# Performance work log

Hardware: AMD Instinct MI355X
Metric: run time of the kernel (lower is better)

Reference implementation:

```python
import jax, jax.numpy as jnp
import numpy as np

NEG = -1e9
CLIP = 10.0  # tanh clipping constant for SingleHeadAttention logits


def layer_norm(x, g, b, eps=1e-5):
    mu = jnp.mean(x, axis=-1, keepdims=True)
    var = jnp.var(x, axis=-1, keepdims=True)
    return (x - mu) * jax.lax.rsqrt(var + eps) * g + b


def setup_inputs() -> dict:
    key = jax.random.key(0)
    ks = jax.random.split(key, 16)
    B, A, N, E, Hf = 4096, 16, 128, 128, 128
    s = 0.02
    inp = {
        "agent_embed": jax.random.normal(ks[0], (B, A, E), jnp.float32),
        "city_embed": jax.random.normal(ks[1], (B, N, E), jnp.float32),
        "acts": jax.random.randint(ks[2], (B, A), 0, N, jnp.int32),
        # cross-attention layer params
        "Wq": jax.random.normal(ks[3], (E, E), jnp.float32) * s,
        "Wk": jax.random.normal(ks[4], (E, E), jnp.float32) * s,
        "Wv": jax.random.normal(ks[5], (E, E), jnp.float32) * s,
        "Wo": jax.random.normal(ks[6], (E, E), jnp.float32) * s,
        "ln1_g": jnp.ones((E,), jnp.float32),
        "ln1_b": jnp.zeros((E,), jnp.float32),
        "W1": jax.random.normal(ks[7], (E, Hf), jnp.float32) * s,
        "b1": jnp.zeros((Hf,), jnp.float32),
        "W2": jax.random.normal(ks[8], (Hf, E), jnp.float32) * s,
        "b2": jnp.zeros((E,), jnp.float32),
        "ln2_g": jnp.ones((E,), jnp.float32),
        "ln2_b": jnp.zeros((E,), jnp.float32),
        # single-head attention params
        "Wq_s": jax.random.normal(ks[9], (E, E), jnp.float32) * s,
        "Wk_s": jax.random.normal(ks[10], (E, E), jnp.float32) * s,
    }
    return inp


def reference(agent_embed, city_embed, acts, Wq, Wk, Wv, Wo, ln1_g, ln1_b,
              W1, b1, W2, b2, ln2_g, ln2_b, Wq_s, Wk_s):
    B, A, E = agent_embed.shape
    H = 8
    dh = E // H

    # ---- conflict mask construction ----
    eq = acts[:, :, None] == acts[:, None, :]            # [B,A,A] True = same city
    ident = jnp.eye(A, dtype=bool)[None]                 # [1,A,A]
    conflict = jnp.where(acts[:, :, None] == 0, ident, eq)
    mask = ~conflict                                     # True = blocked in attention

    # ---- gather per-agent selected city embeddings ----
    selected = jnp.take_along_axis(city_embed, acts[:, :, None].astype(jnp.int32), axis=1)  # [B,A,E]

    # ---- cross-attention layer (num_layers = 1) ----
    cac = selected
    q = (cac @ Wq).reshape(B, A, H, dh)
    k = (agent_embed @ Wk).reshape(B, A, H, dh)
    v = (agent_embed @ Wv).reshape(B, A, H, dh)
    scores = jnp.einsum("bqhd,bkhd->bhqk", q, k) / np.sqrt(dh).astype(np.float32)
    scores = jnp.where(mask[:, None, :, :], NEG, scores)
    attn = jax.nn.softmax(scores, axis=-1)
    out = jnp.einsum("bhqk,bkhd->bqhd", attn, v).reshape(B, A, E) @ Wo
    h = layer_norm(cac + out, ln1_g, ln1_b)
    ffn = jax.nn.relu(h @ W1 + b1) @ W2 + b2
    cac = layer_norm(h + ffn, ln2_g, ln2_b)

    # ---- single-head attention producing logits [B,A,A] ----
    qs = cac @ Wq_s
    ks_ = agent_embed @ Wk_s
    logits = jnp.einsum("bqe,bke->bqk", qs, ks_) / np.sqrt(E).astype(np.float32)
    logits = CLIP * jnp.tanh(logits)
    logits = jnp.where(mask, NEG, logits)
    return logits
```

## Files before the change

kernel.cpp:

```cpp
#include <hip/hip_runtime.h>
#include <hip/hip_bf16.h>
#include <math.h>

typedef __attribute__((ext_vector_type(8))) short bfrag;
typedef __attribute__((ext_vector_type(4))) short short4v;
typedef __attribute__((ext_vector_type(4))) float f32x4;

#define LDK 136


static __device__ __forceinline__ float b2f(short s)
{
    unsigned int u = ((unsigned int)(unsigned short)s) << 16;
    float f;
    __builtin_memcpy(&f, &u, 4);
    return f;
}

__global__ __launch_bounds__(256) void prep_weights(
    const float* __restrict__ Wq, const float* __restrict__ Wk,
    const float* __restrict__ Wv, const float* __restrict__ Wo,
    const float* __restrict__ W1, const float* __restrict__ W2,
    const float* __restrict__ Wqs, const float* __restrict__ Wks,
    __hip_bfloat16* __restrict__ out)
{
    __shared__ __hip_bfloat16 t[128 * 17];
    const float* Ws[8] = {Wq, Wk, Wv, Wo, W1, W2, Wqs, Wks};
    const int mat = blockIdx.x >> 3;
    const int slab = blockIdx.x & 7;
    const float* W = Ws[mat];
    const int n0 = slab * 16;
    __hip_bfloat16* o = out + (size_t)mat * 16384 + (size_t)n0 * 128;

#pragma unroll
    for (int p = 0; p < 2; ++p) {
        int idx = p * 256 + threadIdx.x;
        int k = idx >> 2, c4 = idx & 3;
        float4 f = *(const float4*)(W + k * 128 + n0 + c4 * 4);
        __hip_bfloat16* d = t + k * 17 + c4 * 4;
        d[0] = __float2bfloat16(f.x); d[1] = __float2bfloat16(f.y);
        d[2] = __float2bfloat16(f.z); d[3] = __float2bfloat16(f.w);
    }
    __syncthreads();
    {
        int n = threadIdx.x >> 4;
        int k0 = (threadIdx.x & 15) * 8;
        __hip_bfloat16 v[8];
#pragma unroll
        for (int j = 0; j < 8; ++j) v[j] = t[(k0 + j) * 17 + n];
        *(bfrag*)(o + n * 128 + k0) = *(const bfrag*)v;
    }
}

__device__ __forceinline__ void mm_accT(const __hip_bfloat16* X,
                                        const __hip_bfloat16* __restrict__ wT,
                                        int m, int quad, int ct0, f32x4 acc[2][2])
{
    const f32x4 z = {0.f, 0.f, 0.f, 0.f};
    acc[0][0] = z; acc[0][1] = z; acc[1][0] = z; acc[1][1] = z;
#pragma unroll
    for (int kk = 0; kk < 128; kk += 32) {
        const int k = kk + quad * 8;
        bfrag x0 = *(const bfrag*)(X + m * LDK + k);
        bfrag x1 = *(const bfrag*)(X + (16 + m) * LDK + k);
        bfrag w0 = *(const bfrag*)(wT + (size_t)(ct0 * 16 + m) * 128 + k);
        bfrag w1 = *(const bfrag*)(wT + (size_t)((ct0 + 1) * 16 + m) * 128 + k);
        acc[0][0] = __builtin_amdgcn_mfma_f32_16x16x32_bf16(w0, x0, acc[0][0], 0, 0, 0);
        acc[1][0] = __builtin_amdgcn_mfma_f32_16x16x32_bf16(w0, x1, acc[1][0], 0, 0, 0);
        acc[0][1] = __builtin_amdgcn_mfma_f32_16x16x32_bf16(w1, x0, acc[0][1], 0, 0, 0);
        acc[1][1] = __builtin_amdgcn_mfma_f32_16x16x32_bf16(w1, x1, acc[1][1], 0, 0, 0);
    }
}

__device__ __forceinline__ void mm_acc(const __hip_bfloat16* A,
                                       const __hip_bfloat16* __restrict__ wT,
                                       int m, int quad, int ct0, f32x4 acc[2][2])
{
    const f32x4 z = {0.f, 0.f, 0.f, 0.f};
    acc[0][0] = z; acc[0][1] = z; acc[1][0] = z; acc[1][1] = z;
#pragma unroll
    for (int kk = 0; kk < 128; kk += 32) {
        const int k = kk + quad * 8;
        bfrag a0 = *(const bfrag*)(A + m * LDK + k);
        bfrag a1 = *(const bfrag*)(A + (16 + m) * LDK + k);
        bfrag b0 = *(const bfrag*)(wT + (size_t)(ct0 * 16 + m) * 128 + k);
        bfrag b1 = *(const bfrag*)(wT + (size_t)((ct0 + 1) * 16 + m) * 128 + k);
        acc[0][0] = __builtin_amdgcn_mfma_f32_16x16x32_bf16(a0, b0, acc[0][0], 0, 0, 0);
        acc[1][0] = __builtin_amdgcn_mfma_f32_16x16x32_bf16(a1, b0, acc[1][0], 0, 0, 0);
        acc[0][1] = __builtin_amdgcn_mfma_f32_16x16x32_bf16(a0, b1, acc[0][1], 0, 0, 0);
        acc[1][1] = __builtin_amdgcn_mfma_f32_16x16x32_bf16(a1, b1, acc[1][1], 0, 0, 0);
    }
}

__device__ __forceinline__ void store_t(__hip_bfloat16* dst, f32x4 acc[2][2],
                                        int m, int quad, int ct0)
{
#pragma unroll
    for (int rt = 0; rt < 2; ++rt)
#pragma unroll
        for (int c = 0; c < 2; ++c) {
            __hip_bfloat16 pk[4];
#pragma unroll
            for (int r = 0; r < 4; ++r) pk[r] = __float2bfloat16(acc[rt][c][r]);
            *(short4v*)(dst + (rt * 16 + m) * LDK + (ct0 + c) * 16 + quad * 4) =
                *(const short4v*)pk;
        }
}

__device__ __forceinline__ void ln_step(const __hip_bfloat16* in, __hip_bfloat16* outb,
                                        const float* __restrict__ g,
                                        const float* __restrict__ bb, int tid)
{
    int row = tid >> 3;
    int part = tid & 7;
    const __hip_bfloat16* p = in + row * LDK + part * 16;
    bfrag h0 = *(const bfrag*)p;
    bfrag h1 = *(const bfrag*)(p + 8);
    float x[16];
#pragma unroll
    for (int j = 0; j < 8; ++j) { x[j] = b2f(h0[j]); x[8 + j] = b2f(h1[j]); }
    float s = 0.f, s2 = 0.f;
#pragma unroll
    for (int j = 0; j < 16; ++j) { s += x[j]; s2 += x[j] * x[j]; }
#pragma unroll
    for (int off = 1; off < 8; off <<= 1) {
        s += __shfl_xor(s, off, 64);
        s2 += __shfl_xor(s2, off, 64);
    }
    float mu = s * (1.f / 128.f);
    float var = s2 * (1.f / 128.f) - mu * mu;
    float sc = rsqrtf(var + 1e-5f);
    __hip_bfloat16* o = outb + row * LDK + part * 16;
#pragma unroll
    for (int j4 = 0; j4 < 4; ++j4) {
        float4 g4 = *(const float4*)(g + part * 16 + j4 * 4);
        float4 b4 = *(const float4*)(bb + part * 16 + j4 * 4);
        float gg[4] = {g4.x, g4.y, g4.z, g4.w};
        float bbv[4] = {b4.x, b4.y, b4.z, b4.w};
        __hip_bfloat16 pk[4];
#pragma unroll
        for (int r = 0; r < 4; ++r)
            pk[r] = __float2bfloat16((x[j4 * 4 + r] - mu) * sc * gg[r] + bbv[r]);
        *(short4v*)(o + j4 * 4) = *(const short4v*)pk;
    }
}

__global__ __launch_bounds__(256) void fused_model(
    const float* __restrict__ agent_embed,
    const float* __restrict__ city_embed,
    const int* __restrict__ acts,
    const __hip_bfloat16* __restrict__ wts,
    const float* __restrict__ ln1g, const float* __restrict__ ln1b,
    const float* __restrict__ b1, const float* __restrict__ b2,
    const float* __restrict__ ln2g, const float* __restrict__ ln2b,
    float* __restrict__ out)
{
    __shared__ __align__(16) __hip_bfloat16 sXA[32 * LDK];
    __shared__ __align__(16) __hip_bfloat16 sXS[32 * LDK];
    __shared__ __align__(16) __hip_bfloat16 sK [32 * LDK];
    __shared__ __align__(16) __hip_bfloat16 sV [32 * LDK];
    __shared__ __align__(16) __hip_bfloat16 sKS[32 * LDK];
    __shared__ __align__(16) __hip_bfloat16 sQ [32 * LDK];
    __shared__ int sActs[32];

    const int tid = threadIdx.x;
    const int lane = tid & 63;
    const int wave = tid >> 6;
    const int m = lane & 15;
    const int quad = lane >> 4;
    const int ct0 = wave * 2;
    const int b0 = blockIdx.x * 2;

    if (tid < 32) sActs[tid] = acts[b0 * 16 + tid];
    {
        const float4* src = (const float4*)(agent_embed + (size_t)b0 * 16 * 128);
#pragma unroll
        for (int p = 0; p < 4; ++p) {
            int v = p * 256 + tid;
            float4 f = src[v];
            int flat = v * 4;
            __hip_bfloat16 pk[4];
            pk[0] = __float2bfloat16(f.x); pk[1] = __float2bfloat16(f.y);
            pk[2] = __float2bfloat16(f.z); pk[3] = __float2bfloat16(f.w);
            *(short4v*)(sXA + (flat >> 7) * LDK + (flat & 127)) = *(const short4v*)pk;
        }
    }
    {
        int r = tid >> 3, part = tid & 7;
        int b = b0 + (r >> 4), i = r & 15;
        int act = acts[b * 16 + i];
        const float4* src = (const float4*)(city_embed + ((size_t)b * 128 + act) * 128);
        __hip_bfloat16* d = sXS + r * LDK + part * 16;
#pragma unroll
        for (int p = 0; p < 4; ++p) {
            float4 f = src[part * 4 + p];
            __hip_bfloat16 pk[4];
            pk[0] = __float2bfloat16(f.x); pk[1] = __float2bfloat16(f.y);
            pk[2] = __float2bfloat16(f.z); pk[3] = __float2bfloat16(f.w);
            *(short4v*)(d + p * 4) = *(const short4v*)pk;
        }
    }
    __syncthreads();

    f32x4 acc[2][2];

    mm_accT(sXA, wts + 1 * 16384, m, quad, ct0, acc); store_t(sK, acc, m, quad, ct0);
    mm_acc(sXA, wts + 2 * 16384, m, quad, ct0, acc);
#pragma unroll
    for (int rt = 0; rt < 2; ++rt)
#pragma unroll
        for (int c = 0; c < 2; ++c) {
            __hip_bfloat16 pk[4];
#pragma unroll
            for (int r = 0; r < 4; ++r) pk[r] = __float2bfloat16(acc[rt][c][r]);
            *(short4v*)(sV + ((rt * 8 + ct0 + c) * 16 + m) * 16 + quad * 4) =
                *(const short4v*)pk;
        }
    mm_accT(sXA, wts + 7 * 16384, m, quad, ct0, acc); store_t(sKS, acc, m, quad, ct0);
    mm_accT(sXS, wts + 0 * 16384, m, quad, ct0, acc); store_t(sQ, acc, m, quad, ct0);
    __syncthreads();

    {
        const f32x4 z4 = {0.f, 0.f, 0.f, 0.f};
        const int g = wave >> 1;
        const int aq = sActs[g * 16 + m];
        bool keep[4];
#pragma unroll
        for (int r = 0; r < 4; ++r) {
            int k = quad * 4 + r;
            int ak = sActs[g * 16 + k];
            keep[r] = (aq == 0) ? (k == m) : (ak == aq);
        }
#pragma unroll
        for (int pp = 0; pp < 4; ++pp) {
            const int h = (wave & 1) * 4 + pp;
            short4v kf = *(const short4v*)(sK + (g * 16 + m) * LDK + h * 16 + quad * 4);
            short4v qf = *(const short4v*)(sQ + (g * 16 + m) * LDK + h * 16 + quad * 4);
            f32x4 sc = __builtin_amdgcn_mfma_f32_16x16x16bf16_1k(kf, qf, z4, 0, 0, 0);
            float e[4], s = 0.f;
#pragma unroll
            for (int r = 0; r < 4; ++r) {
                e[r] = keep[r] ? __expf(sc[r] * 0.25f) : 0.f;
                s += e[r];
            }
            s += __shfl_xor(s, 16, 64);
            s += __shfl_xor(s, 32, 64);
            float inv = __builtin_amdgcn_rcpf(s);
            __hip_bfloat16 pk[4];
#pragma unroll
            for (int r = 0; r < 4; ++r) pk[r] = __float2bfloat16(e[r] * inv);
            short4v pa = *(const short4v*)pk;
            short4v vf = *(const short4v*)(sV + ((g * 8 + h) * 16 + m) * 16 + quad * 4);
            f32x4 o4 = __builtin_amdgcn_mfma_f32_16x16x16bf16_1k(pa, vf, z4, 0, 0, 0);
#pragma unroll
            for (int r = 0; r < 4; ++r)
                sXA[(g * 16 + quad * 4 + r) * LDK + h * 16 + m] =
                    __float2bfloat16(o4[r]);
        }
    }
    __syncthreads();

    mm_accT(sXA, wts + 3 * 16384, m, quad, ct0, acc);
#pragma unroll
    for (int rt = 0; rt < 2; ++rt)
#pragma unroll
        for (int c = 0; c < 2; ++c) {
            const int off = (rt * 16 + m) * LDK + (ct0 + c) * 16 + quad * 4;
            short4v sv = *(const short4v*)(sXS + off);
            __hip_bfloat16 pk[4];
#pragma unroll
            for (int r = 0; r < 4; ++r)
                pk[r] = __float2bfloat16(acc[rt][c][r] + b2f(sv[r]));
            *(short4v*)(sQ + off) = *(const short4v*)pk;
        }
    __syncthreads();

    ln_step(sQ, sK, ln1g, ln1b, tid);
    __syncthreads();

    mm_accT(sK, wts + 4 * 16384, m, quad, ct0, acc);
#pragma unroll
    for (int rt = 0; rt < 2; ++rt)
#pragma unroll
        for (int c = 0; c < 2; ++c) {
            float4 bv = *(const float4*)(b1 + (ct0 + c) * 16 + quad * 4);
            float bb4[4] = {bv.x, bv.y, bv.z, bv.w};
            __hip_bfloat16 pk[4];
#pragma unroll
            for (int r = 0; r < 4; ++r)
                pk[r] = __float2bfloat16(fmaxf(acc[rt][c][r] + bb4[r], 0.f));
            *(short4v*)(sV + (rt * 16 + m) * LDK + (ct0 + c) * 16 + quad * 4) =
                *(const short4v*)pk;
        }
    __syncthreads();

    mm_accT(sV, wts + 5 * 16384, m, quad, ct0, acc);
#pragma unroll
    for (int rt = 0; rt < 2; ++rt)
#pragma unroll
        for (int c = 0; c < 2; ++c) {
            const int off = (rt * 16 + m) * LDK + (ct0 + c) * 16 + quad * 4;
            float4 bv = *(const float4*)(b2 + (ct0 + c) * 16 + quad * 4);
            float bb4[4] = {bv.x, bv.y, bv.z, bv.w};
            short4v hv = *(const short4v*)(sK + off);
            __hip_bfloat16 pk[4];
#pragma unroll
            for (int r = 0; r < 4; ++r)
                pk[r] = __float2bfloat16(acc[rt][c][r] + bb4[r] + b2f(hv[r]));
            *(short4v*)(sXA + off) = *(const short4v*)pk;
        }
    __syncthreads();

    ln_step(sXA, sXS, ln2g, ln2b, tid);
    __syncthreads();

    mm_accT(sXS, wts + 6 * 16384, m, quad, ct0, acc);
    store_t(sK, acc, m, quad, ct0);
    __syncthreads();

    if (wave < 2) {
        int g = wave;
        f32x4 la = {0.f, 0.f, 0.f, 0.f};
#pragma unroll
        for (int kk = 0; kk < 128; kk += 32) {
            int k = kk + quad * 8;
            bfrag a = *(const bfrag*)(sK + (g * 16 + m) * LDK + k);
            bfrag b = *(const bfrag*)(sKS + (g * 16 + m) * LDK + k);
            la = __builtin_amdgcn_mfma_f32_16x16x32_bf16(a, b, la, 0, 0, 0);
        }
        int b = b0 + g;
        int kcol = m;
        int ak = sActs[g * 16 + kcol];
#pragma unroll
        for (int r = 0; r < 4; ++r) {
            int q = quad * 4 + r;
            int aq = sActs[g * 16 + q];
            float v = la[r] * 0.0883883476483184f;
            v = 10.f * tanhf(v);
            bool conflict = (aq == 0) ? (q == kcol) : (aq == ak);
            out[((size_t)b * 16 + q) * 16 + kcol] = conflict ? v : -1e9f;
        }
    }
}

extern "C" void kernel_launch(void* const* d_in, const int* in_sizes, int n_in,
                              void* d_out, int out_size, void* d_ws, size_t ws_size,
                              hipStream_t stream)
{
    const float* agent = (const float*)d_in[0];
    const float* city  = (const float*)d_in[1];
    const int*   acts  = (const int*)d_in[2];
    const float* Wq  = (const float*)d_in[3];
    const float* Wk  = (const float*)d_in[4];
    const float* Wv  = (const float*)d_in[5];
    const float* Wo  = (const float*)d_in[6];
    const float* l1g = (const float*)d_in[7];
    const float* l1b = (const float*)d_in[8];
    const float* W1  = (const float*)d_in[9];
    const float* b1  = (const float*)d_in[10];
    const float* W2  = (const float*)d_in[11];
    const float* b2  = (const float*)d_in[12];
    const float* l2g = (const float*)d_in[13];
    const float* l2b = (const float*)d_in[14];
    const float* Wqs = (const float*)d_in[15];
    const float* Wks = (const float*)d_in[16];
    float* out = (float*)d_out;

    int B = in_sizes[2] / 16;
    __hip_bfloat16* wts = (__hip_bfloat16*)d_ws;

    prep_weights<<<64, 256, 0, stream>>>(Wq, Wk, Wv, Wo, W1, W2, Wqs, Wks, wts);
    fused_model<<<B / 2, 256, 0, stream>>>(agent, city, acts, wts, l1g, l1b,
                                           b1, b2, l2g, l2b, out);
}
```

Baseline: 416.3 us.

## Restructure fused kernel to one wave per batch element with register-resident activations

The fused model kernel now launches one 64-thread block per batch element instead of a 256-thread block handling two. Each wave computes all eight 16-column tiles of every projection itself and keeps K, V, Q and intermediate activations in registers as packed bf16 fragments. Shared memory shrinks to a single 16-row scratch buffer used only to transpose the layout between matmuls. This removes block-wide barriers and most LDS traffic and lets LayerNorm reduce with in-wave shuffles. In exchange each wave issues four times more MFMAs and weight loads, and register pressure rises sharply, which may lower occupancy.

```diff
diff --git a/kernel.cpp b/kernel.cpp
--- a/kernel.cpp
+++ b/kernel.cpp
@@ -7,7 +7,6 @@
 typedef __attribute__((ext_vector_type(4))) float f32x4;
 
 #define LDK 136
-
 
 static __device__ __forceinline__ float b2f(short s)
 {
@@ -15,6 +14,39 @@
     float f;
     __builtin_memcpy(&f, &u, 4);
     return f;
+}
+
+static __device__ __forceinline__ short4v pack4(f32x4 a)
+{
+    short4v o;
+#pragma unroll
+    for (int r = 0; r < 4; ++r) {
+        __hip_bfloat16 h = __float2bfloat16(a[r]);
+        short s;
+        __builtin_memcpy(&s, &h, 2);
+        o[r] = s;
+    }
+    return o;
+}
+
+static __device__ __forceinline__ bfrag pack8(f32x4 a, f32x4 b)
+{
+    bfrag o;
+#pragma unroll
+    for (int j = 0; j < 4; ++j) {
+        __hip_bfloat16 h = __float2bfloat16(a[j]);
+        short s;
+        __builtin_memcpy(&s, &h, 2);
+        o[j] = s;
+    }
+#pragma unroll
+    for (int j = 0; j < 4; ++j) {
+        __hip_bfloat16 h = __float2bfloat16(b[j]);
+        short s;
+        __builtin_memcpy(&s, &h, 2);
+        o[4 + j] = s;
+    }
+    return o;
 }
 
 __global__ __launch_bounds__(256) void prep_weights(
@@ -52,100 +84,39 @@
     }
 }
 
-__device__ __forceinline__ void mm_accT(const __hip_bfloat16* X,
-                                        const __hip_bfloat16* __restrict__ wT,
-                                        int m, int quad, int ct0, f32x4 acc[2][2])
+__device__ __forceinline__ void mmT8(const bfrag x[4],
+                                     const __hip_bfloat16* __restrict__ wT,
+                                     int m, int quad, f32x4 acc[8])
 {
     const f32x4 z = {0.f, 0.f, 0.f, 0.f};
-    acc[0][0] = z; acc[0][1] = z; acc[1][0] = z; acc[1][1] = z;
-#pragma unroll
-    for (int kk = 0; kk < 128; kk += 32) {
-        const int k = kk + quad * 8;
-        bfrag x0 = *(const bfrag*)(X + m * LDK + k);
-        bfrag x1 = *(const bfrag*)(X + (16 + m) * LDK + k);
-        bfrag w0 = *(const bfrag*)(wT + (size_t)(ct0 * 16 + m) * 128 + k);
-        bfrag w1 = *(const bfrag*)(wT + (size_t)((ct0 + 1) * 16 + m) * 128 + k);
-        acc[0][0] = __builtin_amdgcn_mfma_f32_16x16x32_bf16(w0, x0, acc[0][0], 0, 0, 0);
-        acc[1][0] = __builtin_amdgcn_mfma_f32_16x16x32_bf16(w0, x1, acc[1][0], 0, 0, 0);
-        acc[0][1] = __builtin_amdgcn_mfma_f32_16x16x32_bf16(w1, x0, acc[0][1], 0, 0, 0);
-        acc[1][1] = __builtin_amdgcn_mfma_f32_16x16x32_bf16(w1, x1, acc[1][1], 0, 0, 0);
-    }
-}
-
-__device__ __forceinline__ void mm_acc(const __hip_bfloat16* A,
-                                       const __hip_bfloat16* __restrict__ wT,
-                                       int m, int quad, int ct0, f32x4 acc[2][2])
+#pragma unroll
+    for (int ct = 0; ct < 8; ++ct) acc[ct] = z;
+#pragma unroll
+    for (int kk = 0; kk < 4; ++kk)
+#pragma unroll
+        for (int ct = 0; ct < 8; ++ct) {
+            bfrag w = *(const bfrag*)(wT + (size_t)(ct * 16 + m) * 128 + kk * 32 + quad * 8);
+            acc[ct] = __builtin_amdgcn_mfma_f32_16x16x32_bf16(w, x[kk], acc[ct], 0, 0, 0);
+        }
+}
+
+__device__ __forceinline__ void mmR8(const bfrag x[4],
+                                     const __hip_bfloat16* __restrict__ wT,
+                                     int m, int quad, f32x4 acc[8])
 {
     const f32x4 z = {0.f, 0.f, 0.f, 0.f};
-    acc[0][0] = z; acc[0][1] = z; acc[1][0] = z; acc[1][1] = z;
-#pragma unroll
-    for (int kk = 0; kk < 128; kk += 32) {
-        const int k = kk + quad * 8;
-        bfrag a0 = *(const bfrag*)(A + m * LDK + k);
-        bfrag a1 = *(const bfrag*)(A + (16 + m) * LDK + k);
-        bfrag b0 = *(const bfrag*)(wT + (size_t)(ct0 * 16 + m) * 128 + k);
-        bfrag b1 = *(const bfrag*)(wT + (size_t)((ct0 + 1) * 16 + m) * 128 + k);
-        acc[0][0] = __builtin_amdgcn_mfma_f32_16x16x32_bf16(a0, b0, acc[0][0], 0, 0, 0);
-        acc[1][0] = __builtin_amdgcn_mfma_f32_16x16x32_bf16(a1, b0, acc[1][0], 0, 0, 0);
-        acc[0][1] = __builtin_amdgcn_mfma_f32_16x16x32_bf16(a0, b1, acc[0][1], 0, 0, 0);
-        acc[1][1] = __builtin_amdgcn_mfma_f32_16x16x32_bf16(a1, b1, acc[1][1], 0, 0, 0);
-    }
-}
-
-__device__ __forceinline__ void store_t(__hip_bfloat16* dst, f32x4 acc[2][2],
-                                        int m, int quad, int ct0)
-{
-#pragma unroll
-    for (int rt = 0; rt < 2; ++rt)
-#pragma unroll
-        for (int c = 0; c < 2; ++c) {
-            __hip_bfloat16 pk[4];
-#pragma unroll
-            for (int r = 0; r < 4; ++r) pk[r] = __float2bfloat16(acc[rt][c][r]);
-            *(short4v*)(dst + (rt * 16 + m) * LDK + (ct0 + c) * 16 + quad * 4) =
-                *(const short4v*)pk;
-        }
-}
-
-__device__ __forceinline__ void ln_step(const __hip_bfloat16* in, __hip_bfloat16* outb,
-                                        const float* __restrict__ g,
-                                        const float* __restrict__ bb, int tid)
-{
-    int row = tid >> 3;
-    int part = tid & 7;
-    const __hip_bfloat16* p = in + row * LDK + part * 16;
-    bfrag h0 = *(const bfrag*)p;
-    bfrag h1 = *(const bfrag*)(p + 8);
-    float x[16];
-#pragma unroll
-    for (int j = 0; j < 8; ++j) { x[j] = b2f(h0[j]); x[8 + j] = b2f(h1[j]); }
-    float s = 0.f, s2 = 0.f;
-#pragma unroll
-    for (int j = 0; j < 16; ++j) { s += x[j]; s2 += x[j] * x[j]; }
-#pragma unroll
-    for (int off = 1; off < 8; off <<= 1) {
-        s += __shfl_xor(s, off, 64);
-        s2 += __shfl_xor(s2, off, 64);
-    }
-    float mu = s * (1.f / 128.f);
-    float var = s2 * (1.f / 128.f) - mu * mu;
-    float sc = rsqrtf(var + 1e-5f);
-    __hip_bfloat16* o = outb + row * LDK + part * 16;
-#pragma unroll
-    for (int j4 = 0; j4 < 4; ++j4) {
-        float4 g4 = *(const float4*)(g + part * 16 + j4 * 4);
-        float4 b4 = *(const float4*)(bb + part * 16 + j4 * 4);
-        float gg[4] = {g4.x, g4.y, g4.z, g4.w};
-        float bbv[4] = {b4.x, b4.y, b4.z, b4.w};
-        __hip_bfloat16 pk[4];
-#pragma unroll
-        for (int r = 0; r < 4; ++r)
-            pk[r] = __float2bfloat16((x[j4 * 4 + r] - mu) * sc * gg[r] + bbv[r]);
-        *(short4v*)(o + j4 * 4) = *(const short4v*)pk;
-    }
-}
-
-__global__ __launch_bounds__(256) void fused_model(
+#pragma unroll
+    for (int ct = 0; ct < 8; ++ct) acc[ct] = z;
+#pragma unroll
+    for (int kk = 0; kk < 4; ++kk)
+#pragma unroll
+        for (int ct = 0; ct < 8; ++ct) {
+            bfrag w = *(const bfrag*)(wT + (size_t)(ct * 16 + m) * 128 + kk * 32 + quad * 8);
+            acc[ct] = __builtin_amdgcn_mfma_f32_16x16x32_bf16(x[kk], w, acc[ct], 0, 0, 0);
+        }
+}
+
+__global__ __launch_bounds__(64) void fused_model(
     const float* __restrict__ agent_embed,
     const float* __restrict__ city_embed,
     const int* __restrict__ acts,
@@ -155,88 +126,59 @@
     const float* __restrict__ ln2g, const float* __restrict__ ln2b,
     float* __restrict__ out)
 {
-    __shared__ __align__(16) __hip_bfloat16 sXA[32 * LDK];
-    __shared__ __align__(16) __hip_bfloat16 sXS[32 * LDK];
-    __shared__ __align__(16) __hip_bfloat16 sK [32 * LDK];
-    __shared__ __align__(16) __hip_bfloat16 sV [32 * LDK];
-    __shared__ __align__(16) __hip_bfloat16 sKS[32 * LDK];
-    __shared__ __align__(16) __hip_bfloat16 sQ [32 * LDK];
-    __shared__ int sActs[32];
-
-    const int tid = threadIdx.x;
-    const int lane = tid & 63;
-    const int wave = tid >> 6;
+    __shared__ __align__(16) __hip_bfloat16 sb[16 * LDK];
+
+    const int lane = threadIdx.x & 63;
     const int m = lane & 15;
     const int quad = lane >> 4;
-    const int ct0 = wave * 2;
-    const int b0 = blockIdx.x * 2;
-
-    if (tid < 32) sActs[tid] = acts[b0 * 16 + tid];
-    {
-        const float4* src = (const float4*)(agent_embed + (size_t)b0 * 16 * 128);
-#pragma unroll
-        for (int p = 0; p < 4; ++p) {
-            int v = p * 256 + tid;
-            float4 f = src[v];
-            int flat = v * 4;
-            __hip_bfloat16 pk[4];
-            pk[0] = __float2bfloat16(f.x); pk[1] = __float2bfloat16(f.y);
-            pk[2] = __float2bfloat16(f.z); pk[3] = __float2bfloat16(f.w);
-            *(short4v*)(sXA + (flat >> 7) * LDK + (flat & 127)) = *(const short4v*)pk;
-        }
-    }
-    {
-        int r = tid >> 3, part = tid & 7;
-        int b = b0 + (r >> 4), i = r & 15;
-        int act = acts[b * 16 + i];
-        const float4* src = (const float4*)(city_embed + ((size_t)b * 128 + act) * 128);
-        __hip_bfloat16* d = sXS + r * LDK + part * 16;
-#pragma unroll
-        for (int p = 0; p < 4; ++p) {
-            float4 f = src[part * 4 + p];
-            __hip_bfloat16 pk[4];
-            pk[0] = __float2bfloat16(f.x); pk[1] = __float2bfloat16(f.y);
-            pk[2] = __float2bfloat16(f.z); pk[3] = __float2bfloat16(f.w);
-            *(short4v*)(d + p * 4) = *(const short4v*)pk;
-        }
-    }
-    __syncthreads();
-
-    f32x4 acc[2][2];
-
-    mm_accT(sXA, wts + 1 * 16384, m, quad, ct0, acc); store_t(sK, acc, m, quad, ct0);
-    mm_acc(sXA, wts + 2 * 16384, m, quad, ct0, acc);
-#pragma unroll
-    for (int rt = 0; rt < 2; ++rt)
-#pragma unroll
-        for (int c = 0; c < 2; ++c) {
-            __hip_bfloat16 pk[4];
-#pragma unroll
-            for (int r = 0; r < 4; ++r) pk[r] = __float2bfloat16(acc[rt][c][r]);
-            *(short4v*)(sV + ((rt * 8 + ct0 + c) * 16 + m) * 16 + quad * 4) =
-                *(const short4v*)pk;
-        }
-    mm_accT(sXA, wts + 7 * 16384, m, quad, ct0, acc); store_t(sKS, acc, m, quad, ct0);
-    mm_accT(sXS, wts + 0 * 16384, m, quad, ct0, acc); store_t(sQ, acc, m, quad, ct0);
-    __syncthreads();
+    const int b = blockIdx.x;
+
+    const int aq = acts[b * 16 + m];
+    bool keep[4];
+#pragma unroll
+    for (int r = 0; r < 4; ++r) {
+        int ak = __shfl(aq, quad * 4 + r, 16);
+        keep[r] = (aq == 0) ? (quad * 4 + r == m) : (ak == aq);
+    }
+
+    const float* arow = agent_embed + ((size_t)b * 16 + m) * 128;
+    const float* crow = city_embed + ((size_t)b * 128 + aq) * 128;
+    bfrag xa[4], xsk[4];
+#pragma unroll
+    for (int kk = 0; kk < 4; ++kk) {
+        f32x4 a0 = *(const f32x4*)(arow + kk * 32 + quad * 8);
+        f32x4 a1 = *(const f32x4*)(arow + kk * 32 + quad * 8 + 4);
+        xa[kk] = pack8(a0, a1);
+        f32x4 c0 = *(const f32x4*)(crow + kk * 32 + quad * 8);
+        f32x4 c1 = *(const f32x4*)(crow + kk * 32 + quad * 8 + 4);
+        xsk[kk] = pack8(c0, c1);
+    }
+    short4v xsr[8];
+#pragma unroll
+    for (int ct = 0; ct < 8; ++ct)
+        xsr[ct] = pack4(*(const f32x4*)(crow + ct * 16 + quad * 4));
+
+    f32x4 acc[8];
+    short4v kf[8], vf[8], ksf[8], qf[8];
+
+    mmT8(xa, wts + 1 * 16384, m, quad, acc);
+#pragma unroll
+    for (int ct = 0; ct < 8; ++ct) kf[ct] = pack4(acc[ct]);
+    mmR8(xa, wts + 2 * 16384, m, quad, acc);
+#pragma unroll
+    for (int ct = 0; ct < 8; ++ct) vf[ct] = pack4(acc[ct]);
+    mmT8(xa, wts + 7 * 16384, m, quad, acc);
+#pragma unroll
+    for (int ct = 0; ct < 8; ++ct) ksf[ct] = pack4(acc[ct]);
+    mmT8(xsk, wts + 0 * 16384, m, quad, acc);
+#pragma unroll
+    for (int ct = 0; ct < 8; ++ct) qf[ct] = pack4(acc[ct]);
 
     {
         const f32x4 z4 = {0.f, 0.f, 0.f, 0.f};
-        const int g = wave >> 1;
-        const int aq = sActs[g * 16 + m];
-        bool keep[4];
-#pragma unroll
-        for (int r = 0; r < 4; ++r) {
-            int k = quad * 4 + r;
-            int ak = sActs[g * 16 + k];
-            keep[r] = (aq == 0) ? (k == m) : (ak == aq);
-        }
-#pragma unroll
-        for (int pp = 0; pp < 4; ++pp) {
-            const int h = (wave & 1) * 4 + pp;
-            short4v kf = *(const short4v*)(sK + (g * 16 + m) * LDK + h * 16 + quad * 4);
-            short4v qf = *(const short4v*)(sQ + (g * 16 + m) * LDK + h * 16 + quad * 4);
-            f32x4 sc = __builtin_amdgcn_mfma_f32_16x16x16bf16_1k(kf, qf, z4, 0, 0, 0);
+#pragma unroll
+        for (int h = 0; h < 8; ++h) {
+            f32x4 sc = __builtin_amdgcn_mfma_f32_16x16x16bf16_1k(kf[h], qf[h], z4, 0, 0, 0);
             float e[4], s = 0.f;
 #pragma unroll
             for (int r = 0; r < 4; ++r) {
@@ -246,100 +188,119 @@
             s += __shfl_xor(s, 16, 64);
             s += __shfl_xor(s, 32, 64);
             float inv = __builtin_amdgcn_rcpf(s);
-            __hip_bfloat16 pk[4];
-#pragma unroll
-            for (int r = 0; r < 4; ++r) pk[r] = __float2bfloat16(e[r] * inv);
-            short4v pa = *(const short4v*)pk;
-            short4v vf = *(const short4v*)(sV + ((g * 8 + h) * 16 + m) * 16 + quad * 4);
-            f32x4 o4 = __builtin_amdgcn_mfma_f32_16x16x16bf16_1k(pa, vf, z4, 0, 0, 0);
-#pragma unroll
-            for (int r = 0; r < 4; ++r)
-                sXA[(g * 16 + quad * 4 + r) * LDK + h * 16 + m] =
-                    __float2bfloat16(o4[r]);
-        }
-    }
-    __syncthreads();
-
-    mm_accT(sXA, wts + 3 * 16384, m, quad, ct0, acc);
-#pragma unroll
-    for (int rt = 0; rt < 2; ++rt)
-#pragma unroll
-        for (int c = 0; c < 2; ++c) {
-            const int off = (rt * 16 + m) * LDK + (ct0 + c) * 16 + quad * 4;
-            short4v sv = *(const short4v*)(sXS + off);
-            __hip_bfloat16 pk[4];
-#pragma unroll
-            for (int r = 0; r < 4; ++r)
-                pk[r] = __float2bfloat16(acc[rt][c][r] + b2f(sv[r]));
-            *(short4v*)(sQ + off) = *(const short4v*)pk;
-        }
-    __syncthreads();
-
-    ln_step(sQ, sK, ln1g, ln1b, tid);
-    __syncthreads();
-
-    mm_accT(sK, wts + 4 * 16384, m, quad, ct0, acc);
-#pragma unroll
-    for (int rt = 0; rt < 2; ++rt)
-#pragma unroll
-        for (int c = 0; c < 2; ++c) {
-            float4 bv = *(const float4*)(b1 + (ct0 + c) * 16 + quad * 4);
-            float bb4[4] = {bv.x, bv.y, bv.z, bv.w};
-            __hip_bfloat16 pk[4];
-#pragma unroll
-            for (int r = 0; r < 4; ++r)
-                pk[r] = __float2bfloat16(fmaxf(acc[rt][c][r] + bb4[r], 0.f));
-            *(short4v*)(sV + (rt * 16 + m) * LDK + (ct0 + c) * 16 + quad * 4) =
-                *(const short4v*)pk;
-        }
-    __syncthreads();
-
-    mm_accT(sV, wts + 5 * 16384, m, quad, ct0, acc);
-#pragma unroll
-    for (int rt = 0; rt < 2; ++rt)
-#pragma unroll
-        for (int c = 0; c < 2; ++c) {
-            const int off = (rt * 16 + m) * LDK + (ct0 + c) * 16 + quad * 4;
-            float4 bv = *(const float4*)(b2 + (ct0 + c) * 16 + quad * 4);
-            float bb4[4] = {bv.x, bv.y, bv.z, bv.w};
-            short4v hv = *(const short4v*)(sK + off);
-            __hip_bfloat16 pk[4];
-#pragma unroll
-            for (int r = 0; r < 4; ++r)
-                pk[r] = __float2bfloat16(acc[rt][c][r] + bb4[r] + b2f(hv[r]));
-            *(short4v*)(sXA + off) = *(const short4v*)pk;
-        }
-    __syncthreads();
-
-    ln_step(sXA, sXS, ln2g, ln2b, tid);
-    __syncthreads();
-
-    mm_accT(sXS, wts + 6 * 16384, m, quad, ct0, acc);
-    store_t(sK, acc, m, quad, ct0);
-    __syncthreads();
-
-    if (wave < 2) {
-        int g = wave;
+            f32x4 p;
+#pragma unroll
+            for (int r = 0; r < 4; ++r) p[r] = e[r] * inv;
+            short4v pa = pack4(p);
+            f32x4 o4 = __builtin_amdgcn_mfma_f32_16x16x16bf16_1k(vf[h], pa, z4, 0, 0, 0);
+            *(short4v*)(sb + m * LDK + h * 16 + quad * 4) = pack4(o4);
+        }
+    }
+    bfrag xo[4];
+#pragma unroll
+    for (int kk = 0; kk < 4; ++kk)
+        xo[kk] = *(const bfrag*)(sb + m * LDK + kk * 32 + quad * 8);
+
+    mmT8(xo, wts + 3 * 16384, m, quad, acc);
+#pragma unroll
+    for (int ct = 0; ct < 8; ++ct)
+#pragma unroll
+        for (int r = 0; r < 4; ++r) acc[ct][r] += b2f(xsr[ct][r]);
+
+    short4v hf[8];
+    {
+        float s = 0.f, s2 = 0.f;
+#pragma unroll
+        for (int ct = 0; ct < 8; ++ct)
+#pragma unroll
+            for (int r = 0; r < 4; ++r) { float v = acc[ct][r]; s += v; s2 += v * v; }
+        s += __shfl_xor(s, 16, 64);  s += __shfl_xor(s, 32, 64);
+        s2 += __shfl_xor(s2, 16, 64); s2 += __shfl_xor(s2, 32, 64);
+        float mu = s * (1.f / 128.f);
+        float var = s2 * (1.f / 128.f) - mu * mu;
+        float rs = rsqrtf(var + 1e-5f);
+#pragma unroll
+        for (int ct = 0; ct < 8; ++ct) {
+            f32x4 g4 = *(const f32x4*)(ln1g + ct * 16 + quad * 4);
+            f32x4 bb4 = *(const f32x4*)(ln1b + ct * 16 + quad * 4);
+            f32x4 hh;
+#pragma unroll
+            for (int r = 0; r < 4; ++r) hh[r] = (acc[ct][r] - mu) * rs * g4[r] + bb4[r];
+            hf[ct] = pack4(hh);
+            *(short4v*)(sb + m * LDK + ct * 16 + quad * 4) = hf[ct];
+        }
+    }
+    bfrag hx[4];
+#pragma unroll
+    for (int kk = 0; kk < 4; ++kk)
+        hx[kk] = *(const bfrag*)(sb + m * LDK + kk * 32 + quad * 8);
+
+    mmT8(hx, wts + 4 * 16384, m, quad, acc);
+#pragma unroll
+    for (int ct = 0; ct < 8; ++ct) {
+        f32x4 bb4 = *(const f32x4*)(b1 + ct * 16 + quad * 4);
+        f32x4 f;
+#pragma unroll
+        for (int r = 0; r < 4; ++r) f[r] = fmaxf(acc[ct][r] + bb4[r], 0.f);
+        *(short4v*)(sb + m * LDK + ct * 16 + quad * 4) = pack4(f);
+    }
+    bfrag fx[4];
+#pragma unroll
+    for (int kk = 0; kk < 4; ++kk)
+        fx[kk] = *(const bfrag*)(sb + m * LDK + kk * 32 + quad * 8);
+
+    mmT8(fx, wts + 5 * 16384, m, quad, acc);
+#pragma unroll
+    for (int ct = 0; ct < 8; ++ct) {
+        f32x4 bb4 = *(const f32x4*)(b2 + ct * 16 + quad * 4);
+#pragma unroll
+        for (int r = 0; r < 4; ++r) acc[ct][r] += bb4[r] + b2f(hf[ct][r]);
+    }
+
+    {
+        float s = 0.f, s2 = 0.f;
+#pragma unroll
+        for (int ct = 0; ct < 8; ++ct)
+#pragma unroll
+            for (int r = 0; r < 4; ++r) { float v = acc[ct][r]; s += v; s2 += v * v; }
+        s += __shfl_xor(s, 16, 64);  s += __shfl_xor(s, 32, 64);
+        s2 += __shfl_xor(s2, 16, 64); s2 += __shfl_xor(s2, 32, 64);
+        float mu = s * (1.f / 128.f);
+        float var = s2 * (1.f / 128.f) - mu * mu;
+        float rs = rsqrtf(var + 1e-5f);
+#pragma unroll
+        for (int ct = 0; ct < 8; ++ct) {
+            f32x4 g4 = *(const f32x4*)(ln2g + ct * 16 + quad * 4);
+            f32x4 bb4 = *(const f32x4*)(ln2b + ct * 16 + quad * 4);
+            f32x4 cc;
+#pragma unroll
+            for (int r = 0; r < 4; ++r) cc[r] = (acc[ct][r] - mu) * rs * g4[r] + bb4[r];
+            *(short4v*)(sb + m * LDK + ct * 16 + quad * 4) = pack4(cc);
+        }
+    }
+    bfrag cx[4];
+#pragma unroll
+    for (int kk = 0; kk < 4; ++kk)
+        cx[kk] = *(const bfrag*)(sb + m * LDK + kk * 32 + quad * 8);
+
+    mmT8(cx, wts + 6 * 16384, m, quad, acc);
+    short4v qsf[8];
+#pragma unroll
+    for (int ct = 0; ct < 8; ++ct) qsf[ct] = pack4(acc[ct]);
+
+    {
         f32x4 la = {0.f, 0.f, 0.f, 0.f};
 #pragma unroll
-        for (int kk = 0; kk < 128; kk += 32) {
-            int k = kk + quad * 8;
-            bfrag a = *(const bfrag*)(sK + (g * 16 + m) * LDK + k);
-            bfrag b = *(const bfrag*)(sKS + (g * 16 + m) * LDK + k);
-            la = __builtin_amdgcn_mfma_f32_16x16x32_bf16(a, b, la, 0, 0, 0);
-        }
-        int b = b0 + g;
-        int kcol = m;
-        int ak = sActs[g * 16 + kcol];
+        for (int ct = 0; ct < 8; ++ct)
+            la = __builtin_amdgcn_mfma_f32_16x16x16bf16_1k(ksf[ct], qsf[ct], la, 0, 0, 0);
+        f32x4 o4;
 #pragma unroll
         for (int r = 0; r < 4; ++r) {
-            int q = quad * 4 + r;
-            int aq = sActs[g * 16 + q];
             float v = la[r] * 0.0883883476483184f;
             v = 10.f * tanhf(v);
-            bool conflict = (aq == 0) ? (q == kcol) : (aq == ak);
-            out[((size_t)b * 16 + q) * 16 + kcol] = conflict ? v : -1e9f;
-        }
+            o4[r] = keep[r] ? v : -1e9f;
+        }
+        *(f32x4*)(out + ((size_t)b * 16 + m) * 16 + quad * 4) = o4;
     }
 }
 
@@ -370,6 +331,6 @@
     __hip_bfloat16* wts = (__hip_bfloat16*)d_ws;
 
     prep_weights<<<64, 256, 0, stream>>>(Wq, Wk, Wv, Wo, W1, W2, Wqs, Wks, wts);
-    fused_model<<<B / 2, 256, 0, stream>>>(agent, city, acts, wts, l1g, l1b,
-                                           b1, b2, l2g, l2b, out);
-}
+    fused_model<<<B, 64, 0, stream>>>(agent, city, acts, wts, l1g, l1b,
+                                      b1, b2, l2g, l2b, out);
+}
```

After: 469.6 us. 1.13x slower.
